# Optimization experiments

Hardware: AMD Instinct MI355X
Metric: run time of the kernel (lower is better)

Reference implementation:

```python
import jax, jax.numpy as jnp
import numpy as np

N, E, F, H, C = 10000, 640000, 128, 128, 40


def setup_inputs() -> dict:
    key = jax.random.key(0)
    ks = jax.random.split(key, 4)
    x = jax.random.normal(ks[0], (N, F), dtype=jnp.float32)
    edge_index = jax.random.randint(ks[1], (2, E), 0, N, dtype=jnp.int64)
    W1 = jax.random.normal(ks[2], (F, H), dtype=jnp.float32) * (1.0 / np.sqrt(F))
    b1 = jnp.zeros((H,), dtype=jnp.float32)
    W2 = jax.random.normal(ks[3], (H, C), dtype=jnp.float32) * (1.0 / np.sqrt(H))
    b2 = jnp.zeros((C,), dtype=jnp.float32)
    return {"x": x, "edge_index": edge_index, "W1": W1, "b1": b1, "W2": W2, "b2": b2}


def _gcn_norm(edge_index, n):
    # PyG GCNConv default: add self-loops, symmetric D^-1/2 (A+I) D^-1/2 norm.
    loop = jnp.arange(n, dtype=edge_index.dtype)
    src = jnp.concatenate([edge_index[0], loop])
    dst = jnp.concatenate([edge_index[1], loop])
    deg = jax.ops.segment_sum(jnp.ones_like(src, dtype=jnp.float32), dst, num_segments=n)
    dinv = jnp.where(deg > 0, jax.lax.rsqrt(deg), 0.0)
    norm = dinv[src] * dinv[dst]  # [E+N]
    return src, dst, norm


def _gcn_conv(h, src, dst, norm, W, b, n):
    hm = h @ W                                   # transform first (smaller dim ok)
    msg = hm[src] * norm[:, None]                # gather + scale  [E+N, out]
    out = jax.ops.segment_sum(msg, dst, num_segments=n)  # scatter-add
    return out + b


def reference(x, edge_index, W1, b1, W2, b2):
    n = x.shape[0]
    src, dst, norm = _gcn_norm(edge_index, n)
    h = jax.nn.relu(_gcn_conv(x, src, dst, norm, W1, b1, n))
    # dropout p=0.5 is identity in eval mode
    out = _gcn_conv(h, src, dst, norm, W2, b2, n)
    return out
```

## Files before the change

### kernel.cpp

```cpp
#include <hip/hip_runtime.h>
#include <hip/hip_fp16.h>


#define FEAT 128
#define CHUNK_LOG 13
#define CHUNK (1 << CHUNK_LOG)
#define G2S 48

__device__ __forceinline__ int load_idx(const void* p, long long i, int is64) {
  if (is64) return (int)((const long long*)p)[i];
  return ((const int*)p)[i];
}

__device__ __forceinline__ int detect_is64(const void* edges) {
  long long v = ((const long long*)edges)[threadIdx.x & 63];
  return __ballot(v < 0 || v >= (1LL << 32)) == 0ULL;
}

__global__ void count_gemm1_kernel(const void* edges, long long E, int nchunk,
                                   unsigned short* __restrict__ counts, int ncp,
                                   unsigned short* __restrict__ rank,
                                   const float* __restrict__ x,
                                   const float* __restrict__ W1,
                                   float* __restrict__ hm1, int n) {
  if ((int)blockIdx.x < nchunk) {
    extern __shared__ unsigned int hist[];
    int is64 = detect_is64(edges);
    int q = blockIdx.x;
    int nw = (n + 1) >> 1;
    for (int i = threadIdx.x; i < nw; i += blockDim.x) hist[i] = 0;
    __syncthreads();
    long long base = (long long)q << CHUNK_LOG;
    long long rem = E - base;
    int m = (rem < (long long)CHUNK) ? (int)rem : CHUNK;
    for (int t = threadIdx.x; t < m; t += blockDim.x) {
      long long e = base + t;
      int dst = load_idx(edges, E + e, is64);
      int sh = (dst & 1) << 4;
      unsigned int old = atomicAdd(&hist[dst >> 1], 1u << sh);
      rank[e] = (unsigned short)((old >> sh) & 0xffffu);
    }
    __syncthreads();
    for (int i = threadIdx.x; i < nw; i += blockDim.x) {
      unsigned int v = hist[i];
      int node0 = i << 1;
      counts[(long long)node0 * ncp + q] = (unsigned short)(v & 0xffffu);
      if (node0 + 1 < n)
        counts[(long long)(node0 + 1) * ncp + q] = (unsigned short)(v >> 16);
    }
  } else {
    int tid = ((int)blockIdx.x - nchunk) * (int)blockDim.x + (int)threadIdx.x;
    int n4 = (n + 3) >> 2;
    if (tid >= n4 * 32) return;
    int i4 = tid >> 5;
    int j = (tid & 31) << 2;
    int r0 = i4 << 2;
    const float* xr = x + (long long)r0 * FEAT;
    if (r0 + 4 <= n) {
      float4 a0 = {0.f,0.f,0.f,0.f}, a1 = a0, a2 = a0, a3 = a0;
      #pragma unroll 4
      for (int k = 0; k < FEAT; ++k) {
        float4 w = *(const float4*)(W1 + k * FEAT + j);
        float x0 = xr[k];
        float x1 = xr[FEAT + k];
        float x2 = xr[2 * FEAT + k];
        float x3 = xr[3 * FEAT + k];
        a0.x = fmaf(x0, w.x, a0.x); a0.y = fmaf(x0, w.y, a0.y);
        a0.z = fmaf(x0, w.z, a0.z); a0.w = fmaf(x0, w.w, a0.w);
        a1.x = fmaf(x1, w.x, a1.x); a1.y = fmaf(x1, w.y, a1.y);
        a1.z = fmaf(x1, w.z, a1.z); a1.w = fmaf(x1, w.w, a1.w);
        a2.x = fmaf(x2, w.x, a2.x); a2.y = fmaf(x2, w.y, a2.y);
        a2.z = fmaf(x2, w.z, a2.z); a2.w = fmaf(x2, w.w, a2.w);
        a3.x = fmaf(x3, w.x, a3.x); a3.y = fmaf(x3, w.y, a3.y);
        a3.z = fmaf(x3, w.z, a3.z); a3.w = fmaf(x3, w.w, a3.w);
      }
      *(float4*)(hm1 + (long long)(r0 + 0) * FEAT + j) = a0;
      *(float4*)(hm1 + (long long)(r0 + 1) * FEAT + j) = a1;
      *(float4*)(hm1 + (long long)(r0 + 2) * FEAT + j) = a2;
      *(float4*)(hm1 + (long long)(r0 + 3) * FEAT + j) = a3;
    } else {
      for (int r = 0; r0 + r < n; ++r) {
        float4 a = {0.f,0.f,0.f,0.f};
        for (int k = 0; k < FEAT; ++k) {
          float4 w = *(const float4*)(W1 + k * FEAT + j);
          float xv = xr[(long long)r * FEAT + k];
          a.x = fmaf(xv, w.x, a.x); a.y = fmaf(xv, w.y, a.y);
          a.z = fmaf(xv, w.z, a.z); a.w = fmaf(xv, w.w, a.w);
        }
        *(float4*)(hm1 + (long long)(r0 + r) * FEAT + j) = a;
      }
    }
  }
}

__global__ void prefix_kernel(unsigned short* counts, int ncp, int* deg,
                              float* dinv, int n, int nchunk) {
  int i = (int)((blockIdx.x * (long long)blockDim.x + threadIdx.x) >> 6);
  int lane = threadIdx.x & 63;
  int nw32 = (nchunk + 1) >> 1;
  if (i >= n) return;
  if (nw32 <= 64) {
    unsigned int* r32 = (unsigned int*)(counts + (long long)i * ncp);
    unsigned int v = (lane < nw32) ? r32[lane] : 0u;
    int q0 = lane << 1;
    int c0 = (q0 < nchunk) ? (int)(v & 0xffffu) : 0;
    int c1 = (q0 + 1 < nchunk) ? (int)(v >> 16) : 0;
    int s = c0 + c1;
    int run = s;
    #pragma unroll
    for (int off = 1; off < 64; off <<= 1) {
      int t = __shfl_up(run, off);
      if (lane >= off) run += t;
    }
    int excl = run - s;
    if (lane < nw32)
      r32[lane] = (unsigned int)(excl & 0xffff) |
                  ((unsigned int)((excl + c0) & 0xffff) << 16);
    if (lane == 63) {
      deg[i] = run;
      dinv[i] = rsqrtf((float)run + 1.0f);
    }
  } else {
    if (lane == 0) {
      int run = 0;
      for (int q = 0; q < nchunk; ++q) {
        long long idx = (long long)i * ncp + q;
        int c = counts[idx];
        counts[idx] = (unsigned short)run;
        run += c;
      }
      deg[i] = run;
      dinv[i] = rsqrtf((float)run + 1.0f);
    }
  }
}

__global__ void scan_scale_kernel(const int* __restrict__ deg, int* row_ptr,
                                  const float* __restrict__ hm1,
                                  __half* __restrict__ g1h,
                                  const float* __restrict__ dinv, int n) {
  if (blockIdx.x == 0) {
    __shared__ int wsum[16];
    int t = threadIdx.x;
    int lane = t & 63, wid = t >> 6;
    int K = (n + 1023) >> 10;
    int base = t * K;
    int s = 0;
    for (int i = 0; i < K; ++i) { int idx = base + i; if (idx < n) s += deg[idx]; }
    int incl = s;
    #pragma unroll
    for (int off = 1; off < 64; off <<= 1) {
      int tmp = __shfl_up(incl, off);
      if (lane >= off) incl += tmp;
    }
    if (lane == 63) wsum[wid] = incl;
    __syncthreads();
    if (wid == 0) {
      int w = (lane < 16) ? wsum[lane] : 0;
      #pragma unroll
      for (int off = 1; off < 16; off <<= 1) {
        int tmp = __shfl_up(w, off);
        if (lane >= off) w += tmp;
      }
      if (lane < 16) wsum[lane] = w;
    }
    __syncthreads();
    int wbase = (wid > 0) ? wsum[wid - 1] : 0;
    int run = wbase + incl - s;
    for (int i = 0; i < K; ++i) {
      int idx = base + i;
      if (idx < n) { row_ptr[idx] = run; run += deg[idx]; }
    }
    if (t == 1023) row_ptr[n] = wsum[15];
  } else {
    int tid = ((int)blockIdx.x - 1) * (int)blockDim.x + (int)threadIdx.x;
    int row = tid >> 5;
    int j = (tid & 31) << 2;
    if (row > n) return;
    if (row < n) {
      float di = dinv[row];
      float4 v = *(const float4*)(hm1 + (long long)row * FEAT + j);
      union { __half2 h2[2]; uint2 u; } pk;
      pk.h2[0] = __floats2half2_rn(v.x * di, v.y * di);
      pk.h2[1] = __floats2half2_rn(v.z * di, v.w * di);
      *(uint2*)(g1h + (long long)row * FEAT + j) = pk.u;
    } else {
      uint2 z = {0u, 0u};
      *(uint2*)(g1h + (long long)n * FEAT + j) = z;
    }
  }
}

__global__ void fill_kernel(const void* edges, long long E,
                            const int* __restrict__ row_ptr,
                            const unsigned short* __restrict__ counts, int ncp,
                            const unsigned short* __restrict__ rank,
                            unsigned short* __restrict__ csr) {
  int is64 = detect_is64(edges);
  long long e = blockIdx.x * (long long)blockDim.x + threadIdx.x;
  if (e >= E) return;
  int r = (int)(e >> CHUNK_LOG);
  int s = load_idx(edges, e, is64);
  int d = load_idx(edges, E + e, is64);
  int pos = row_ptr[d] + (int)counts[(long long)d * ncp + r] + (int)rank[e];
  csr[pos] = (unsigned short)s;
}

__global__ void agg1g2_kernel(const __half* __restrict__ g,
                              const float* __restrict__ dinv,
                              const int* __restrict__ row_ptr,
                              const unsigned short* __restrict__ csr,
                              const float* __restrict__ b1,
                              const float* __restrict__ W2,
                              float* __restrict__ G2, int n, int C) {
  __shared__ float hs[4][FEAT];
  int lane = threadIdx.x & 63;
  int wid = threadIdx.x >> 6;
  int node = ((int)blockIdx.x << 2) | wid;
  if (node < n) {
    const unsigned int* gu = (const unsigned int*)g;
    int beg = row_ptr[node], end = row_ptr[node + 1];
    float ax = 0.f, ay = 0.f;
    for (int base = beg; base < end; base += 64) {
      int ed = (base + lane < end) ? (int)csr[base + lane] : n;
      int m = end - base; if (m > 64) m = 64;
      int mm = (m + 15) & ~15;
      for (int j = 0; j < mm; j += 16) {
        int ss[16];
        unsigned int vv[16];
        #pragma unroll
        for (int p = 0; p < 16; ++p) ss[p] = __shfl(ed, j + p);
        #pragma unroll
        for (int p = 0; p < 16; ++p) vv[p] = gu[(ss[p] << 6) + lane];
        #pragma unroll
        for (int p = 0; p < 16; ++p) {
          float2 v = __half22float2(*(__half2*)&vv[p]);
          ax += v.x; ay += v.y;
        }
      }
    }
    float di = dinv[node];
    float2 self = __half22float2(((const __half2*)g)[(node << 6) + lane]);
    ax += self.x; ay += self.y;
    int f = lane << 1;
    ax = fmaxf(ax * di + b1[f], 0.f);
    ay = fmaxf(ay * di + b1[f + 1], 0.f);
    float2* hp = (float2*)&hs[wid][f];
    *hp = make_float2(ax, ay);
  }
  __syncthreads();
  if (node < n) {
    if (lane < C) {
      const float* hr = hs[wid];
      float acc = 0.f;
      #pragma unroll 8
      for (int k = 0; k < FEAT; ++k)
        acc = fmaf(hr[k], W2[k * C + lane], acc);
      G2[node * G2S + lane] = acc * dinv[node];
    }
  } else if (node == n && lane < C) {
    G2[n * G2S + lane] = 0.f;
  }
}

__global__ void agg2_kernel(const float* __restrict__ G2, const float* __restrict__ dinv,
                            const int* __restrict__ row_ptr,
                            const unsigned short* __restrict__ csr,
                            const float* __restrict__ b2, float* __restrict__ out,
                            int n, int C) {
  int node = (int)((blockIdx.x * (long long)blockDim.x + threadIdx.x) >> 6);
  int lane = threadIdx.x & 63;
  if (node >= n) return;
  int beg = row_ptr[node], end = row_ptr[node + 1];
  float acc = 0.f;
  for (int base = beg; base < end; base += 64) {
    int ed = (base + lane < end) ? (int)csr[base + lane] : n;
    int m = end - base; if (m > 64) m = 64;
    int mm = (m + 15) & ~15;
    for (int j = 0; j < mm; j += 16) {
      int ss[16];
      float vv[16];
      #pragma unroll
      for (int p = 0; p < 16; ++p) ss[p] = __shfl(ed, j + p);
      #pragma unroll
      for (int p = 0; p < 16; ++p)
        vv[p] = (lane < C) ? G2[(long long)ss[p] * G2S + lane] : 0.f;
      #pragma unroll
      for (int p = 0; p < 16; ++p) acc += vv[p];
    }
  }
  if (lane < C) {
    float di = dinv[node];
    acc += G2[(long long)node * G2S + lane];
    out[(long long)node * C + lane] = acc * di + b2[lane];
  }
}

extern "C" void kernel_launch(void* const* d_in, const int* in_sizes, int n_in,
                              void* d_out, int out_size, void* d_ws, size_t ws_size,
                              hipStream_t stream) {
  const float* x     = (const float*)d_in[0];
  const void*  edges = d_in[1];
  const float* W1    = (const float*)d_in[2];
  const float* b1    = (const float*)d_in[3];
  const float* W2    = (const float*)d_in[4];
  const float* b2    = (const float*)d_in[5];
  float* out = (float*)d_out;

  const int n = in_sizes[0] / FEAT;
  const long long E = in_sizes[1] / 2;
  const int C = in_sizes[5];
  const int nchunk = (int)((E + CHUNK - 1) >> CHUNK_LOG);
  const int ncp = (nchunk + 1) & ~1;

  char* ws = (char*)d_ws;
  size_t off = 0;
  auto alloc = [&](size_t bytes) -> void* {
    void* p = ws + off;
    off = (off + bytes + 255) & ~(size_t)255;
    return p;
  };
  unsigned short* counts = (unsigned short*)alloc(2ll * ncp * n);
  unsigned short* rank   = (unsigned short*)alloc(2ll * E);
  unsigned short* csr    = (unsigned short*)alloc(2ll * E);
  int*   deg     = (int*)alloc(4ll * n);
  int*   row_ptr = (int*)alloc(4ll * (n + 1));
  float* dinv    = (float*)alloc(4ll * n);
  float* hm1     = (float*)alloc(4ll * n * FEAT);
  __half* g1h    = (__half*)alloc(2ll * (n + 1) * FEAT);
  float* G2      = (float*)alloc(4ll * (n + 1) * G2S);

  int blocksE = (int)((E + 255) / 256);
  int n4 = (n + 3) >> 2;
  int gemmBlocks = (n4 * 32 + 255) / 256;
  int scaleBlocks = ((n + 1) * 32 + 1023) / 1024;
  size_t ldsBytes = (size_t)((n + 1) >> 1) * 4;

  count_gemm1_kernel<<<nchunk + gemmBlocks, 256, ldsBytes, stream>>>(
      edges, E, nchunk, counts, ncp, rank, x, W1, hm1, n);
  prefix_kernel<<<(int)(((long long)n * 64 + 255) / 256), 256, 0, stream>>>(
      counts, ncp, deg, dinv, n, nchunk);
  scan_scale_kernel<<<1 + scaleBlocks, 1024, 0, stream>>>(deg, row_ptr, hm1, g1h,
                                                          dinv, n);
  fill_kernel<<<blocksE, 256, 0, stream>>>(edges, E, row_ptr, counts, ncp, rank, csr);
  int aggBlocks = (n + 4) >> 2;
  agg1g2_kernel<<<aggBlocks, 256, 0, stream>>>(g1h, dinv, row_ptr, csr, b1, W2,
                                               G2, n, C);
  agg2_kernel<<<(n4 * 256 + 255) / 256, 256, 0, stream>>>(G2, dinv, row_ptr, csr,
                                                          b2, out, n, C);
}
```

Baseline: 89.50 us.

## Fuse prefix, scan/scale and CSR fill into one cooperative kernel

Merges three separate launches (per-node chunk prefix, row_ptr scan plus fp16 scaling, CSR fill) into a single cooperative kernel with grid-stride loops, separated by grid.sync barriers. The aim is to remove two kernel launch gaps and their tail drain. In exchange the grid is fixed at 1024 blocks, so each phase loses parallelism and grid-wide barrier overhead is added. The single-block scan now runs on 256 threads instead of 1024.

Result: slower. 279.5 us (+212.2%).

```diff
diff --git a/kernel.cpp b/kernel.cpp
--- a/kernel.cpp
+++ b/kernel.cpp
@@ -1,5 +1,8 @@
 #include <hip/hip_runtime.h>
 #include <hip/hip_fp16.h>
+#include <hip/hip_cooperative_groups.h>
+
+namespace cg = cooperative_groups;
 
 
 #define FEAT 128
@@ -93,35 +96,44 @@
   }
 }
 
-__global__ void prefix_kernel(unsigned short* counts, int ncp, int* deg,
-                              float* dinv, int n, int nchunk) {
-  int i = (int)((blockIdx.x * (long long)blockDim.x + threadIdx.x) >> 6);
+__global__ void __launch_bounds__(256, 4)
+build_kernel(unsigned short* __restrict__ counts, int ncp,
+             int* __restrict__ deg, float* __restrict__ dinv,
+             int* __restrict__ row_ptr,
+             const float* __restrict__ hm1, __half* __restrict__ g1h,
+             const void* edges, long long E,
+             const unsigned short* __restrict__ rank,
+             unsigned short* __restrict__ csr, int n, int nchunk) {
+  cg::grid_group grid = cg::this_grid();
+  int is64 = detect_is64(edges);
   int lane = threadIdx.x & 63;
+  int gwave = (int)((blockIdx.x * (long long)blockDim.x + threadIdx.x) >> 6);
+  int nwaves = (int)(((long long)gridDim.x * blockDim.x) >> 6);
   int nw32 = (nchunk + 1) >> 1;
-  if (i >= n) return;
-  if (nw32 <= 64) {
-    unsigned int* r32 = (unsigned int*)(counts + (long long)i * ncp);
-    unsigned int v = (lane < nw32) ? r32[lane] : 0u;
-    int q0 = lane << 1;
-    int c0 = (q0 < nchunk) ? (int)(v & 0xffffu) : 0;
-    int c1 = (q0 + 1 < nchunk) ? (int)(v >> 16) : 0;
-    int s = c0 + c1;
-    int run = s;
-    #pragma unroll
-    for (int off = 1; off < 64; off <<= 1) {
-      int t = __shfl_up(run, off);
-      if (lane >= off) run += t;
-    }
-    int excl = run - s;
-    if (lane < nw32)
-      r32[lane] = (unsigned int)(excl & 0xffff) |
-                  ((unsigned int)((excl + c0) & 0xffff) << 16);
-    if (lane == 63) {
-      deg[i] = run;
-      dinv[i] = rsqrtf((float)run + 1.0f);
-    }
-  } else {
-    if (lane == 0) {
+
+  for (int i = gwave; i < n; i += nwaves) {
+    if (nw32 <= 64) {
+      unsigned int* r32 = (unsigned int*)(counts + (long long)i * ncp);
+      unsigned int v = (lane < nw32) ? r32[lane] : 0u;
+      int q0 = lane << 1;
+      int c0 = (q0 < nchunk) ? (int)(v & 0xffffu) : 0;
+      int c1 = (q0 + 1 < nchunk) ? (int)(v >> 16) : 0;
+      int s = c0 + c1;
+      int run = s;
+      #pragma unroll
+      for (int off = 1; off < 64; off <<= 1) {
+        int t = __shfl_up(run, off);
+        if (lane >= off) run += t;
+      }
+      int excl = run - s;
+      if (lane < nw32)
+        r32[lane] = (unsigned int)(excl & 0xffff) |
+                    ((unsigned int)((excl + c0) & 0xffff) << 16);
+      if (lane == 63) {
+        deg[i] = run;
+        dinv[i] = rsqrtf((float)run + 1.0f);
+      }
+    } else if (lane == 0) {
       int run = 0;
       for (int q = 0; q < nchunk; ++q) {
         long long idx = (long long)i * ncp + q;
@@ -133,17 +145,13 @@
       dinv[i] = rsqrtf((float)run + 1.0f);
     }
   }
-}
-
-__global__ void scan_scale_kernel(const int* __restrict__ deg, int* row_ptr,
-                                  const float* __restrict__ hm1,
-                                  __half* __restrict__ g1h,
-                                  const float* __restrict__ dinv, int n) {
+  grid.sync();
+
   if (blockIdx.x == 0) {
-    __shared__ int wsum[16];
+    __shared__ int wsum[4];
     int t = threadIdx.x;
-    int lane = t & 63, wid = t >> 6;
-    int K = (n + 1023) >> 10;
+    int wid = t >> 6;
+    int K = (n + 255) >> 8;
     int base = t * K;
     int s = 0;
     for (int i = 0; i < K; ++i) { int idx = base + i; if (idx < n) s += deg[idx]; }
@@ -156,13 +164,13 @@
     if (lane == 63) wsum[wid] = incl;
     __syncthreads();
     if (wid == 0) {
-      int w = (lane < 16) ? wsum[lane] : 0;
-      #pragma unroll
-      for (int off = 1; off < 16; off <<= 1) {
+      int w = (lane < 4) ? wsum[lane] : 0;
+      #pragma unroll
+      for (int off = 1; off < 4; off <<= 1) {
         int tmp = __shfl_up(w, off);
         if (lane >= off) w += tmp;
       }
-      if (lane < 16) wsum[lane] = w;
+      if (lane < 4) wsum[lane] = w;
     }
     __syncthreads();
     int wbase = (wid > 0) ? wsum[wid - 1] : 0;
@@ -171,39 +179,38 @@
       int idx = base + i;
       if (idx < n) { row_ptr[idx] = run; run += deg[idx]; }
     }
-    if (t == 1023) row_ptr[n] = wsum[15];
+    if (t == 255) row_ptr[n] = wsum[3];
   } else {
     int tid = ((int)blockIdx.x - 1) * (int)blockDim.x + (int)threadIdx.x;
-    int row = tid >> 5;
-    int j = (tid & 31) << 2;
-    if (row > n) return;
-    if (row < n) {
-      float di = dinv[row];
-      float4 v = *(const float4*)(hm1 + (long long)row * FEAT + j);
-      union { __half2 h2[2]; uint2 u; } pk;
-      pk.h2[0] = __floats2half2_rn(v.x * di, v.y * di);
-      pk.h2[1] = __floats2half2_rn(v.z * di, v.w * di);
-      *(uint2*)(g1h + (long long)row * FEAT + j) = pk.u;
-    } else {
-      uint2 z = {0u, 0u};
-      *(uint2*)(g1h + (long long)n * FEAT + j) = z;
-    }
-  }
-}
-
-__global__ void fill_kernel(const void* edges, long long E,
-                            const int* __restrict__ row_ptr,
-                            const unsigned short* __restrict__ counts, int ncp,
-                            const unsigned short* __restrict__ rank,
-                            unsigned short* __restrict__ csr) {
-  int is64 = detect_is64(edges);
-  long long e = blockIdx.x * (long long)blockDim.x + threadIdx.x;
-  if (e >= E) return;
-  int r = (int)(e >> CHUNK_LOG);
-  int s = load_idx(edges, e, is64);
-  int d = load_idx(edges, E + e, is64);
-  int pos = row_ptr[d] + (int)counts[(long long)d * ncp + r] + (int)rank[e];
-  csr[pos] = (unsigned short)s;
+    int stride = ((int)gridDim.x - 1) * (int)blockDim.x;
+    int total = (n + 1) * 32;
+    for (; tid < total; tid += stride) {
+      int row = tid >> 5;
+      int j = (tid & 31) << 2;
+      if (row < n) {
+        float di = dinv[row];
+        float4 v = *(const float4*)(hm1 + (long long)row * FEAT + j);
+        union { __half2 h2[2]; uint2 u; } pk;
+        pk.h2[0] = __floats2half2_rn(v.x * di, v.y * di);
+        pk.h2[1] = __floats2half2_rn(v.z * di, v.w * di);
+        *(uint2*)(g1h + (long long)row * FEAT + j) = pk.u;
+      } else {
+        uint2 z = {0u, 0u};
+        *(uint2*)(g1h + (long long)n * FEAT + j) = z;
+      }
+    }
+  }
+  grid.sync();
+
+  long long tid0 = blockIdx.x * (long long)blockDim.x + threadIdx.x;
+  long long gsz = (long long)gridDim.x * blockDim.x;
+  for (long long e = tid0; e < E; e += gsz) {
+    int r = (int)(e >> CHUNK_LOG);
+    int s = load_idx(edges, e, is64);
+    int d = load_idx(edges, E + e, is64);
+    int pos = row_ptr[d] + (int)counts[(long long)d * ncp + r] + (int)rank[e];
+    csr[pos] = (unsigned short)s;
+  }
 }
 
 __global__ void agg1g2_kernel(const __half* __restrict__ g,
@@ -330,19 +337,22 @@
   __half* g1h    = (__half*)alloc(2ll * (n + 1) * FEAT);
   float* G2      = (float*)alloc(4ll * (n + 1) * G2S);
 
-  int blocksE = (int)((E + 255) / 256);
   int n4 = (n + 3) >> 2;
   int gemmBlocks = (n4 * 32 + 255) / 256;
-  int scaleBlocks = ((n + 1) * 32 + 1023) / 1024;
   size_t ldsBytes = (size_t)((n + 1) >> 1) * 4;
 
   count_gemm1_kernel<<<nchunk + gemmBlocks, 256, ldsBytes, stream>>>(
       edges, E, nchunk, counts, ncp, rank, x, W1, hm1, n);
-  prefix_kernel<<<(int)(((long long)n * 64 + 255) / 256), 256, 0, stream>>>(
-      counts, ncp, deg, dinv, n, nchunk);
-  scan_scale_kernel<<<1 + scaleBlocks, 1024, 0, stream>>>(deg, row_ptr, hm1, g1h,
-                                                          dinv, n);
-  fill_kernel<<<blocksE, 256, 0, stream>>>(edges, E, row_ptr, counts, ncp, rank, csr);
+
+  {
+    void* args[] = {(void*)&counts, (void*)&ncp, (void*)&deg, (void*)&dinv,
+                    (void*)&row_ptr, (void*)&hm1, (void*)&g1h, (void*)&edges,
+                    (void*)&E, (void*)&rank, (void*)&csr, (void*)&n,
+                    (void*)&nchunk};
+    hipLaunchCooperativeKernel((void*)build_kernel, dim3(1024), dim3(256),
+                               args, 0, stream);
+  }
+
   int aggBlocks = (n + 4) >> 2;
   agg1g2_kernel<<<aggBlocks, 256, 0, stream>>>(g1h, dinv, row_ptr, csr, b1, W2,
                                                G2, n, C);
```

## Replace chunked LDS histogram CSR build with global atomic degree count and cursor fill

Applied to the files above, without the earlier changes.

Drops the per-chunk shared-memory histogram, the rank and counts arrays, and the prefix kernel. Degrees are now counted with global atomics inside the GEMM kernel via a grid-stride loop, and the CSR fill takes slots from per-node cursors with atomicAdd. dinv is computed inside the scale kernel. This removes one kernel launch and a lot of intermediate memory traffic, but adds global atomic contention and makes the neighbor order within each CSR row nondeterministic, which can change float summation order.

Result: slower. 156.3 us (+74.6%).

```diff
diff --git a/kernel.cpp b/kernel.cpp
--- a/kernel.cpp
+++ b/kernel.cpp
@@ -3,8 +3,6 @@
 
 
 #define FEAT 128
-#define CHUNK_LOG 13
-#define CHUNK (1 << CHUNK_LOG)
 #define G2S 48
 
 __device__ __forceinline__ int load_idx(const void* p, long long i, int is64) {
@@ -17,128 +15,66 @@
   return __ballot(v < 0 || v >= (1LL << 32)) == 0ULL;
 }
 
-__global__ void count_gemm1_kernel(const void* edges, long long E, int nchunk,
-                                   unsigned short* __restrict__ counts, int ncp,
-                                   unsigned short* __restrict__ rank,
+__global__ void count_gemm1_kernel(const void* edges, long long E,
+                                   int* __restrict__ deg,
                                    const float* __restrict__ x,
                                    const float* __restrict__ W1,
                                    float* __restrict__ hm1, int n) {
-  if ((int)blockIdx.x < nchunk) {
-    extern __shared__ unsigned int hist[];
-    int is64 = detect_is64(edges);
-    int q = blockIdx.x;
-    int nw = (n + 1) >> 1;
-    for (int i = threadIdx.x; i < nw; i += blockDim.x) hist[i] = 0;
-    __syncthreads();
-    long long base = (long long)q << CHUNK_LOG;
-    long long rem = E - base;
-    int m = (rem < (long long)CHUNK) ? (int)rem : CHUNK;
-    for (int t = threadIdx.x; t < m; t += blockDim.x) {
-      long long e = base + t;
-      int dst = load_idx(edges, E + e, is64);
-      int sh = (dst & 1) << 4;
-      unsigned int old = atomicAdd(&hist[dst >> 1], 1u << sh);
-      rank[e] = (unsigned short)((old >> sh) & 0xffffu);
-    }
-    __syncthreads();
-    for (int i = threadIdx.x; i < nw; i += blockDim.x) {
-      unsigned int v = hist[i];
-      int node0 = i << 1;
-      counts[(long long)node0 * ncp + q] = (unsigned short)(v & 0xffffu);
-      if (node0 + 1 < n)
-        counts[(long long)(node0 + 1) * ncp + q] = (unsigned short)(v >> 16);
-    }
+  int is64 = detect_is64(edges);
+  long long t0 = blockIdx.x * (long long)blockDim.x + threadIdx.x;
+  long long gsz = (long long)gridDim.x * blockDim.x;
+  for (long long e = t0; e < E; e += gsz) {
+    int dst = load_idx(edges, E + e, is64);
+    atomicAdd(&deg[dst], 1);
+  }
+  int tid = (int)t0;
+  int n4 = (n + 3) >> 2;
+  if (tid >= n4 * 32) return;
+  int i4 = tid >> 5;
+  int j = (tid & 31) << 2;
+  int r0 = i4 << 2;
+  const float* xr = x + (long long)r0 * FEAT;
+  if (r0 + 4 <= n) {
+    float4 a0 = {0.f,0.f,0.f,0.f}, a1 = a0, a2 = a0, a3 = a0;
+    #pragma unroll 4
+    for (int k = 0; k < FEAT; ++k) {
+      float4 w = *(const float4*)(W1 + k * FEAT + j);
+      float x0 = xr[k];
+      float x1 = xr[FEAT + k];
+      float x2 = xr[2 * FEAT + k];
+      float x3 = xr[3 * FEAT + k];
+      a0.x = fmaf(x0, w.x, a0.x); a0.y = fmaf(x0, w.y, a0.y);
+      a0.z = fmaf(x0, w.z, a0.z); a0.w = fmaf(x0, w.w, a0.w);
+      a1.x = fmaf(x1, w.x, a1.x); a1.y = fmaf(x1, w.y, a1.y);
+      a1.z = fmaf(x1, w.z, a1.z); a1.w = fmaf(x1, w.w, a1.w);
+      a2.x = fmaf(x2, w.x, a2.x); a2.y = fmaf(x2, w.y, a2.y);
+      a2.z = fmaf(x2, w.z, a2.z); a2.w = fmaf(x2, w.w, a2.w);
+      a3.x = fmaf(x3, w.x, a3.x); a3.y = fmaf(x3, w.y, a3.y);
+      a3.z = fmaf(x3, w.z, a3.z); a3.w = fmaf(x3, w.w, a3.w);
+    }
+    *(float4*)(hm1 + (long long)(r0 + 0) * FEAT + j) = a0;
+    *(float4*)(hm1 + (long long)(r0 + 1) * FEAT + j) = a1;
+    *(float4*)(hm1 + (long long)(r0 + 2) * FEAT + j) = a2;
+    *(float4*)(hm1 + (long long)(r0 + 3) * FEAT + j) = a3;
   } else {
-    int tid = ((int)blockIdx.x - nchunk) * (int)blockDim.x + (int)threadIdx.x;
-    int n4 = (n + 3) >> 2;
-    if (tid >= n4 * 32) return;
-    int i4 = tid >> 5;
-    int j = (tid & 31) << 2;
-    int r0 = i4 << 2;
-    const float* xr = x + (long long)r0 * FEAT;
-    if (r0 + 4 <= n) {
-      float4 a0 = {0.f,0.f,0.f,0.f}, a1 = a0, a2 = a0, a3 = a0;
-      #pragma unroll 4
+    for (int r = 0; r0 + r < n; ++r) {
+      float4 a = {0.f,0.f,0.f,0.f};
       for (int k = 0; k < FEAT; ++k) {
         float4 w = *(const float4*)(W1 + k * FEAT + j);
-        float x0 = xr[k];
-        float x1 = xr[FEAT + k];
-        float x2 = xr[2 * FEAT + k];
-        float x3 = xr[3 * FEAT + k];
-        a0.x = fmaf(x0, w.x, a0.x); a0.y = fmaf(x0, w.y, a0.y);
-        a0.z = fmaf(x0, w.z, a0.z); a0.w = fmaf(x0, w.w, a0.w);
-        a1.x = fmaf(x1, w.x, a1.x); a1.y = fmaf(x1, w.y, a1.y);
-        a1.z = fmaf(x1, w.z, a1.z); a1.w = fmaf(x1, w.w, a1.w);
-        a2.x = fmaf(x2, w.x, a2.x); a2.y = fmaf(x2, w.y, a2.y);
-        a2.z = fmaf(x2, w.z, a2.z); a2.w = fmaf(x2, w.w, a2.w);
-        a3.x = fmaf(x3, w.x, a3.x); a3.y = fmaf(x3, w.y, a3.y);
-        a3.z = fmaf(x3, w.z, a3.z); a3.w = fmaf(x3, w.w, a3.w);
+        float xv = xr[(long long)r * FEAT + k];
+        a.x = fmaf(xv, w.x, a.x); a.y = fmaf(xv, w.y, a.y);
+        a.z = fmaf(xv, w.z, a.z); a.w = fmaf(xv, w.w, a.w);
       }
-      *(float4*)(hm1 + (long long)(r0 + 0) * FEAT + j) = a0;
-      *(float4*)(hm1 + (long long)(r0 + 1) * FEAT + j) = a1;
-      *(float4*)(hm1 + (long long)(r0 + 2) * FEAT + j) = a2;
-      *(float4*)(hm1 + (long long)(r0 + 3) * FEAT + j) = a3;
-    } else {
-      for (int r = 0; r0 + r < n; ++r) {
-        float4 a = {0.f,0.f,0.f,0.f};
-        for (int k = 0; k < FEAT; ++k) {
-          float4 w = *(const float4*)(W1 + k * FEAT + j);
-          float xv = xr[(long long)r * FEAT + k];
-          a.x = fmaf(xv, w.x, a.x); a.y = fmaf(xv, w.y, a.y);
-          a.z = fmaf(xv, w.z, a.z); a.w = fmaf(xv, w.w, a.w);
-        }
-        *(float4*)(hm1 + (long long)(r0 + r) * FEAT + j) = a;
-      }
-    }
-  }
-}
-
-__global__ void prefix_kernel(unsigned short* counts, int ncp, int* deg,
-                              float* dinv, int n, int nchunk) {
-  int i = (int)((blockIdx.x * (long long)blockDim.x + threadIdx.x) >> 6);
-  int lane = threadIdx.x & 63;
-  int nw32 = (nchunk + 1) >> 1;
-  if (i >= n) return;
-  if (nw32 <= 64) {
-    unsigned int* r32 = (unsigned int*)(counts + (long long)i * ncp);
-    unsigned int v = (lane < nw32) ? r32[lane] : 0u;
-    int q0 = lane << 1;
-    int c0 = (q0 < nchunk) ? (int)(v & 0xffffu) : 0;
-    int c1 = (q0 + 1 < nchunk) ? (int)(v >> 16) : 0;
-    int s = c0 + c1;
-    int run = s;
-    #pragma unroll
-    for (int off = 1; off < 64; off <<= 1) {
-      int t = __shfl_up(run, off);
-      if (lane >= off) run += t;
-    }
-    int excl = run - s;
-    if (lane < nw32)
-      r32[lane] = (unsigned int)(excl & 0xffff) |
-                  ((unsigned int)((excl + c0) & 0xffff) << 16);
-    if (lane == 63) {
-      deg[i] = run;
-      dinv[i] = rsqrtf((float)run + 1.0f);
-    }
-  } else {
-    if (lane == 0) {
-      int run = 0;
-      for (int q = 0; q < nchunk; ++q) {
-        long long idx = (long long)i * ncp + q;
-        int c = counts[idx];
-        counts[idx] = (unsigned short)run;
-        run += c;
-      }
-      deg[i] = run;
-      dinv[i] = rsqrtf((float)run + 1.0f);
+      *(float4*)(hm1 + (long long)(r0 + r) * FEAT + j) = a;
     }
   }
 }
 
 __global__ void scan_scale_kernel(const int* __restrict__ deg, int* row_ptr,
+                                  int* __restrict__ cursor,
                                   const float* __restrict__ hm1,
                                   __half* __restrict__ g1h,
-                                  const float* __restrict__ dinv, int n) {
+                                  float* __restrict__ dinv, int n) {
   if (blockIdx.x == 0) {
     __shared__ int wsum[16];
     int t = threadIdx.x;
@@ -169,7 +105,7 @@
     int run = wbase + incl - s;
     for (int i = 0; i < K; ++i) {
       int idx = base + i;
-      if (idx < n) { row_ptr[idx] = run; run += deg[idx]; }
+      if (idx < n) { row_ptr[idx] = run; cursor[idx] = run; run += deg[idx]; }
     }
     if (t == 1023) row_ptr[n] = wsum[15];
   } else {
@@ -178,7 +114,8 @@
     int j = (tid & 31) << 2;
     if (row > n) return;
     if (row < n) {
-      float di = dinv[row];
+      float di = rsqrtf((float)deg[row] + 1.0f);
+      if ((tid & 31) == 0) dinv[row] = di;
       float4 v = *(const float4*)(hm1 + (long long)row * FEAT + j);
       union { __half2 h2[2]; uint2 u; } pk;
       pk.h2[0] = __floats2half2_rn(v.x * di, v.y * di);
@@ -192,17 +129,14 @@
 }
 
 __global__ void fill_kernel(const void* edges, long long E,
-                            const int* __restrict__ row_ptr,
-                            const unsigned short* __restrict__ counts, int ncp,
-                            const unsigned short* __restrict__ rank,
+                            int* __restrict__ cursor,
                             unsigned short* __restrict__ csr) {
   int is64 = detect_is64(edges);
   long long e = blockIdx.x * (long long)blockDim.x + threadIdx.x;
   if (e >= E) return;
-  int r = (int)(e >> CHUNK_LOG);
   int s = load_idx(edges, e, is64);
   int d = load_idx(edges, E + e, is64);
-  int pos = row_ptr[d] + (int)counts[(long long)d * ncp + r] + (int)rank[e];
+  int pos = atomicAdd(&cursor[d], 1);
   csr[pos] = (unsigned short)s;
 }
 
@@ -310,8 +244,6 @@
   const int n = in_sizes[0] / FEAT;
   const long long E = in_sizes[1] / 2;
   const int C = in_sizes[5];
-  const int nchunk = (int)((E + CHUNK - 1) >> CHUNK_LOG);
-  const int ncp = (nchunk + 1) & ~1;
 
   char* ws = (char*)d_ws;
   size_t off = 0;
@@ -320,29 +252,25 @@
     off = (off + bytes + 255) & ~(size_t)255;
     return p;
   };
-  unsigned short* counts = (unsigned short*)alloc(2ll * ncp * n);
-  unsigned short* rank   = (unsigned short*)alloc(2ll * E);
-  unsigned short* csr    = (unsigned short*)alloc(2ll * E);
+  unsigned short* csr = (unsigned short*)alloc(2ll * E);
   int*   deg     = (int*)alloc(4ll * n);
   int*   row_ptr = (int*)alloc(4ll * (n + 1));
+  int*   cursor  = (int*)alloc(4ll * (n + 1));
   float* dinv    = (float*)alloc(4ll * n);
   float* hm1     = (float*)alloc(4ll * n * FEAT);
   __half* g1h    = (__half*)alloc(2ll * (n + 1) * FEAT);
   float* G2      = (float*)alloc(4ll * (n + 1) * G2S);
 
-  int blocksE = (int)((E + 255) / 256);
   int n4 = (n + 3) >> 2;
   int gemmBlocks = (n4 * 32 + 255) / 256;
   int scaleBlocks = ((n + 1) * 32 + 1023) / 1024;
-  size_t ldsBytes = (size_t)((n + 1) >> 1) * 4;
-
-  count_gemm1_kernel<<<nchunk + gemmBlocks, 256, ldsBytes, stream>>>(
-      edges, E, nchunk, counts, ncp, rank, x, W1, hm1, n);
-  prefix_kernel<<<(int)(((long long)n * 64 + 255) / 256), 256, 0, stream>>>(
-      counts, ncp, deg, dinv, n, nchunk);
-  scan_scale_kernel<<<1 + scaleBlocks, 1024, 0, stream>>>(deg, row_ptr, hm1, g1h,
-                                                          dinv, n);
-  fill_kernel<<<blocksE, 256, 0, stream>>>(edges, E, row_ptr, counts, ncp, rank, csr);
+  int blocksE = (int)((E + 255) / 256);
+
+  hipMemsetAsync(deg, 0, 4ll * n, stream);
+  count_gemm1_kernel<<<gemmBlocks, 256, 0, stream>>>(edges, E, deg, x, W1, hm1, n);
+  scan_scale_kernel<<<1 + scaleBlocks, 1024, 0, stream>>>(deg, row_ptr, cursor,
+                                                          hm1, g1h, dinv, n);
+  fill_kernel<<<blocksE, 256, 0, stream>>>(edges, E, cursor, csr);
   int aggBlocks = (n + 4) >> 2;
   agg1g2_kernel<<<aggBlocks, 256, 0, stream>>>(g1h, dinv, row_ptr, csr, b1, W2,
                                                G2, n, C);
```

## Simplify GEMM1 to one row per thread group and prefetch next CSR batch

Applied to the files above, without the earlier changes.

The first-layer GEMM branch drops the 4-row register blocking and has each group of 32 threads compute one output row, so it launches four times as many blocks with less register pressure but reloads W1 more often. Both aggregation kernels now load the next 64-edge batch of CSR indices before processing the current one, hiding index-load latency for high-degree nodes. The prefetch costs one extra register and a load that is guarded and harmless for nodes with at most 64 edges.

Result: slower. 99.86 us (+11.6%).

```diff
diff --git a/kernel.cpp b/kernel.cpp
--- a/kernel.cpp
+++ b/kernel.cpp
@@ -50,46 +50,19 @@
     }
   } else {
     int tid = ((int)blockIdx.x - nchunk) * (int)blockDim.x + (int)threadIdx.x;
-    int n4 = (n + 3) >> 2;
-    if (tid >= n4 * 32) return;
-    int i4 = tid >> 5;
+    if (tid >= n * 32) return;
+    int i = tid >> 5;
     int j = (tid & 31) << 2;
-    int r0 = i4 << 2;
-    const float* xr = x + (long long)r0 * FEAT;
-    if (r0 + 4 <= n) {
-      float4 a0 = {0.f,0.f,0.f,0.f}, a1 = a0, a2 = a0, a3 = a0;
-      #pragma unroll 4
-      for (int k = 0; k < FEAT; ++k) {
-        float4 w = *(const float4*)(W1 + k * FEAT + j);
-        float x0 = xr[k];
-        float x1 = xr[FEAT + k];
-        float x2 = xr[2 * FEAT + k];
-        float x3 = xr[3 * FEAT + k];
-        a0.x = fmaf(x0, w.x, a0.x); a0.y = fmaf(x0, w.y, a0.y);
-        a0.z = fmaf(x0, w.z, a0.z); a0.w = fmaf(x0, w.w, a0.w);
-        a1.x = fmaf(x1, w.x, a1.x); a1.y = fmaf(x1, w.y, a1.y);
-        a1.z = fmaf(x1, w.z, a1.z); a1.w = fmaf(x1, w.w, a1.w);
-        a2.x = fmaf(x2, w.x, a2.x); a2.y = fmaf(x2, w.y, a2.y);
-        a2.z = fmaf(x2, w.z, a2.z); a2.w = fmaf(x2, w.w, a2.w);
-        a3.x = fmaf(x3, w.x, a3.x); a3.y = fmaf(x3, w.y, a3.y);
-        a3.z = fmaf(x3, w.z, a3.z); a3.w = fmaf(x3, w.w, a3.w);
-      }
-      *(float4*)(hm1 + (long long)(r0 + 0) * FEAT + j) = a0;
-      *(float4*)(hm1 + (long long)(r0 + 1) * FEAT + j) = a1;
-      *(float4*)(hm1 + (long long)(r0 + 2) * FEAT + j) = a2;
-      *(float4*)(hm1 + (long long)(r0 + 3) * FEAT + j) = a3;
-    } else {
-      for (int r = 0; r0 + r < n; ++r) {
-        float4 a = {0.f,0.f,0.f,0.f};
-        for (int k = 0; k < FEAT; ++k) {
-          float4 w = *(const float4*)(W1 + k * FEAT + j);
-          float xv = xr[(long long)r * FEAT + k];
-          a.x = fmaf(xv, w.x, a.x); a.y = fmaf(xv, w.y, a.y);
-          a.z = fmaf(xv, w.z, a.z); a.w = fmaf(xv, w.w, a.w);
-        }
-        *(float4*)(hm1 + (long long)(r0 + r) * FEAT + j) = a;
-      }
-    }
+    const float* xr = x + (long long)i * FEAT;
+    float4 a = {0.f, 0.f, 0.f, 0.f};
+    #pragma unroll 8
+    for (int k = 0; k < FEAT; ++k) {
+      float4 w = *(const float4*)(W1 + k * FEAT + j);
+      float xv = xr[k];
+      a.x = fmaf(xv, w.x, a.x); a.y = fmaf(xv, w.y, a.y);
+      a.z = fmaf(xv, w.z, a.z); a.w = fmaf(xv, w.w, a.w);
+    }
+    *(float4*)(hm1 + (long long)i * FEAT + j) = a;
   }
 }
 
@@ -221,8 +194,10 @@
     const unsigned int* gu = (const unsigned int*)g;
     int beg = row_ptr[node], end = row_ptr[node + 1];
     float ax = 0.f, ay = 0.f;
+    int ed = (beg + lane < end) ? (int)csr[beg + lane] : n;
     for (int base = beg; base < end; base += 64) {
-      int ed = (base + lane < end) ? (int)csr[base + lane] : n;
+      int nb = base + 64;
+      int edn = (nb < end && nb + lane < end) ? (int)csr[nb + lane] : n;
       int m = end - base; if (m > 64) m = 64;
       int mm = (m + 15) & ~15;
       for (int j = 0; j < mm; j += 16) {
@@ -238,6 +213,7 @@
           ax += v.x; ay += v.y;
         }
       }
+      ed = edn;
     }
     float di = dinv[node];
     float2 self = __half22float2(((const __half2*)g)[(node << 6) + lane]);
@@ -273,8 +249,10 @@
   if (node >= n) return;
   int beg = row_ptr[node], end = row_ptr[node + 1];
   float acc = 0.f;
+  int ed = (beg + lane < end) ? (int)csr[beg + lane] : n;
   for (int base = beg; base < end; base += 64) {
-    int ed = (base + lane < end) ? (int)csr[base + lane] : n;
+    int nb = base + 64;
+    int edn = (nb < end && nb + lane < end) ? (int)csr[nb + lane] : n;
     int m = end - base; if (m > 64) m = 64;
     int mm = (m + 15) & ~15;
     for (int j = 0; j < mm; j += 16) {
@@ -288,6 +266,7 @@
       #pragma unroll
       for (int p = 0; p < 16; ++p) acc += vv[p];
     }
+    ed = edn;
   }
   if (lane < C) {
     float di = dinv[node];
@@ -330,10 +309,10 @@
   __half* g1h    = (__half*)alloc(2ll * (n + 1) * FEAT);
   float* G2      = (float*)alloc(4ll * (n + 1) * G2S);
 
+  int n4 = (n + 3) >> 2;
+  int gemmBlocks = (n * 32 + 255) / 256;
+  int scaleBlocks = ((n + 1) * 32 + 1023) / 1024;
   int blocksE = (int)((E + 255) / 256);
-  int n4 = (n + 3) >> 2;
-  int gemmBlocks = (n4 * 32 + 255) / 256;
-  int scaleBlocks = ((n + 1) * 32 + 1023) / 1024;
   size_t ldsBytes = (size_t)((n + 1) >> 1) * 4;
 
   count_gemm1_kernel<<<nchunk + gemmBlocks, 256, ldsBytes, stream>>>(
```
